# Kernel optimization log

Measured on AMD Instinct MI355X. Metric: run time of the kernel, lower is better.

The kernel has to match this reference:

```python
import jax, jax.numpy as jnp
import numpy as np

HIDDEN = 2048
N_HEADS = 32
N_KV = 8
HEAD_DIM = HIDDEN // N_HEADS
SEQ = 2048
BATCH = 1
THETA = 10000.0
EPS = 1e-5


def _layernorm(x, g, b):
    mu = jnp.mean(x, axis=-1, keepdims=True)
    var = jnp.var(x, axis=-1, keepdims=True)
    return (x - mu) * jax.lax.rsqrt(var + EPS) * g + b


def _rope_tables(seq_len, dim, theta):
    inv_freq = 1.0 / (theta ** (jnp.arange(0, dim, 2, dtype=jnp.float32) / dim))
    t = jnp.arange(seq_len, dtype=jnp.float32)
    freqs = jnp.einsum('i,j->ij', t, inv_freq)          # [S, D/2]
    emb = jnp.concatenate([freqs, freqs], axis=-1)       # [S, D]
    return jnp.cos(emb), jnp.sin(emb)


def _rotate_half(x):
    x1, x2 = jnp.split(x, 2, axis=-1)
    return jnp.concatenate([-x2, x1], axis=-1)


def setup_inputs() -> dict:
    key = jax.random.key(0)
    ks = jax.random.split(key, 10)
    s = 0.02
    return {
        'x':   jax.random.normal(ks[0], (BATCH, SEQ, HIDDEN), jnp.float32),
        'Wq':  jax.random.normal(ks[1], (HIDDEN, HIDDEN), jnp.float32) * s,
        'bq':  jnp.zeros((HIDDEN,), jnp.float32),
        'Wk':  jax.random.normal(ks[2], (HIDDEN, N_KV * HEAD_DIM), jnp.float32) * s,
        'bk':  jnp.zeros((N_KV * HEAD_DIM,), jnp.float32),
        'Wv':  jax.random.normal(ks[3], (HIDDEN, N_KV * HEAD_DIM), jnp.float32) * s,
        'bv':  jnp.zeros((N_KV * HEAD_DIM,), jnp.float32),
        'Wo':  jax.random.normal(ks[4], (HIDDEN, HIDDEN), jnp.float32) * s,
        'bo':  jnp.zeros((HIDDEN,), jnp.float32),
        'q_g': jnp.ones((HEAD_DIM,), jnp.float32),
        'q_b': jnp.zeros((HEAD_DIM,), jnp.float32),
        'k_g': jnp.ones((HEAD_DIM,), jnp.float32),
        'k_b': jnp.zeros((HEAD_DIM,), jnp.float32),
    }


def reference(x, Wq, bq, Wk, bk, Wv, bv, Wo, bo, q_g, q_b, k_g, k_b):
    B, S, H = x.shape
    n_rep = N_HEADS // N_KV
    # projections
    q = (x @ Wq + bq).reshape(B, S, N_HEADS, HEAD_DIM).transpose(0, 2, 1, 3)  # [B,Hq,S,D]
    k = (x @ Wk + bk).reshape(B, S, N_KV, HEAD_DIM).transpose(0, 2, 1, 3)     # [B,Hkv,S,D]
    v = (x @ Wv + bv).reshape(B, S, N_KV, HEAD_DIM).transpose(0, 2, 1, 3)
    # per-head QK layernorm
    q = _layernorm(q, q_g, q_b)
    k = _layernorm(k, k_g, k_b)
    # RoPE
    cos, sin = _rope_tables(S, HEAD_DIM, THETA)  # [S, D]
    q = q * cos + _rotate_half(q) * sin
    k = k * cos + _rotate_half(k) * sin
    # GQA attention without materializing repeated k/v:
    # repeat_interleave groups adjacent q-heads per kv head -> reshape q to [B,Hkv,rep,S,D]
    qg = q.reshape(B, N_KV, n_rep, S, HEAD_DIM)
    scores = jnp.einsum('bgrqd,bgkd->bgrqk', qg, k) / jnp.sqrt(jnp.float32(HEAD_DIM))
    attn = jax.nn.softmax(scores, axis=-1)
    out = jnp.einsum('bgrqk,bgkd->bgrqd', attn, v)  # [B,Hkv,rep,S,D]
    out = out.reshape(B, N_HEADS, S, HEAD_DIM).transpose(0, 2, 1, 3).reshape(B, S, H)
    return out @ Wo + bo
```

## Files before the change

### kernel.cpp

```cpp
#include <hip/hip_runtime.h>
#include <hip/hip_bf16.h>
#include <stdint.h>

#define S_LEN 2048
#define HID   2048
#define NH    32
#define NKV   8
#define HD    64

typedef __attribute__((ext_vector_type(8))) short bf16x8;
typedef __attribute__((ext_vector_type(4))) float f32x4;
typedef __attribute__((ext_vector_type(16))) float f32x16;

__device__ __forceinline__ short f2bf(float f) {
  __hip_bfloat16 h = __float2bfloat16(f);
  return __builtin_bit_cast(short, h);
}
__device__ __forceinline__ float bf2f(short s) {
  unsigned u = ((unsigned)(unsigned short)s) << 16;
  return __builtin_bit_cast(float, u);
}
__device__ __forceinline__ int cvt_pk_bf16(float lo, float hi) {
  int r;
  asm("v_cvt_pk_bf16_f32 %0, %1, %2" : "=v"(r) : "v"(lo), "v"(hi));
  return r;
}

__global__ void cast_bf16_kernel(const float* __restrict__ in, short* __restrict__ out, int n4) {
  int i = blockIdx.x * blockDim.x + threadIdx.x;
  if (i < n4) {
    float4 v = reinterpret_cast<const float4*>(in)[i];
    short4 o;
    o.x = f2bf(v.x); o.y = f2bf(v.y); o.z = f2bf(v.z); o.w = f2bf(v.w);
    reinterpret_cast<short4*>(out)[i] = o;
  }
}

__global__ void transpose_cast_kernel(const float* __restrict__ in, short* __restrict__ out,
                                      int K, int N) {
  __shared__ float tile[64][65];
  const int k0 = blockIdx.x * 64;
  const int n0 = blockIdx.y * 64;
  const int tn = threadIdx.x & 63;
  const int t4 = threadIdx.x >> 6;
#pragma unroll
  for (int i = 0; i < 16; i++)
    tile[t4 + i * 4][tn] = in[(size_t)(k0 + t4 + i * 4) * N + n0 + tn];
  __syncthreads();
#pragma unroll
  for (int i = 0; i < 16; i++)
    out[(size_t)(n0 + t4 + i * 4) * K + k0 + tn] = f2bf(tile[tn][t4 + i * 4]);
}

__global__ void concat_bias_kernel(const float* __restrict__ bq, const float* __restrict__ bk,
                                   const float* __restrict__ bv, float* __restrict__ out) {
  int i = blockIdx.x * blockDim.x + threadIdx.x;
  if (i < 3072) {
    float v = (i < 2048) ? bq[i] : (i < 2560 ? bk[i - 2048] : bv[i - 2560]);
    out[i] = v;
  }
}

__global__ void rope_table_kernel(float* __restrict__ ctab, float* __restrict__ stab) {
  int i = blockIdx.x * blockDim.x + threadIdx.x;
  if (i < S_LEN * 32) {
    int t = i >> 5, j = i & 31;
    float ang = (float)t * powf(10000.0f, -(float)j / 32.0f);
    ctab[i] = cosf(ang);
    stab[i] = sinf(ang);
  }
}

template <int F32OUT>
__global__ __launch_bounds__(256, 3) void gemm_v2_kernel(
    const short* __restrict__ A, const short* __restrict__ Bt,
    const float* __restrict__ bias, void* __restrict__ Cv,
    int N, int K) {
  __shared__ short Als[2][64 * 64];
  __shared__ short Bls[2][128 * 64];
  const int tid = threadIdx.x;
  const int l = tid & 63, w = tid >> 6;
  const int lg = l >> 4, lc = l & 15;
  const int wr = w >> 1, wc = w & 1;

  const int nwg = gridDim.x;
  const int cpx = nwg >> 3;
  const int swz = (blockIdx.x & 7) * cpx + (blockIdx.x >> 3);
  const int m0 = (swz & 31) << 6;
  const int n0 = (swz >> 5) << 7;

  const int NT = K >> 6;
  const f32x4 zero4 = {0.f, 0.f, 0.f, 0.f};
  f32x4 acc[2][4];
#pragma unroll
  for (int i = 0; i < 2; i++)
#pragma unroll
    for (int j = 0; j < 4; j++) acc[i][j] = zero4;

  const int lrow = l >> 3;
  const int lcol = (l & 7) << 3;

  auto stage = [&](int buf, int kt) {
    const int kofs = kt << 6;
#pragma unroll
    for (int i = 0; i < 2; i++) {
      const short* gsrc = A + (size_t)(m0 + i * 32 + (w << 3) + lrow) * K + kofs + lcol;
      __builtin_amdgcn_global_load_lds(
          (const __attribute__((address_space(1))) unsigned*)gsrc,
          (__attribute__((address_space(3))) unsigned*)(&Als[buf][(i * 32 + (w << 3)) << 6]),
          16, 0, 0);
    }
#pragma unroll
    for (int i = 0; i < 4; i++) {
      const short* gsrc = Bt + (size_t)(n0 + i * 32 + (w << 3) + lrow) * K + kofs + lcol;
      __builtin_amdgcn_global_load_lds(
          (const __attribute__((address_space(1))) unsigned*)gsrc,
          (__attribute__((address_space(3))) unsigned*)(&Bls[buf][(i * 32 + (w << 3)) << 6]),
          16, 0, 0);
    }
  };

  stage(0, 0);
  int cur = 0;
  for (int kt = 0; kt < NT; kt++) {
    __syncthreads();
    if (kt + 1 < NT) stage(cur ^ 1, kt + 1);
    const char* AB = reinterpret_cast<const char*>(Als[cur]);
    const char* BB = reinterpret_cast<const char*>(Bls[cur]);
#pragma unroll
    for (int ks = 0; ks < 2; ks++) {
      bf16x8 af[2], bfr[4];
#pragma unroll
      for (int mi = 0; mi < 2; mi++)
        af[mi] = *reinterpret_cast<const bf16x8*>(
            AB + (wr * 32 + mi * 16 + lc) * 128 + ks * 64 + lg * 16);
#pragma unroll
      for (int nf = 0; nf < 4; nf++)
        bfr[nf] = *reinterpret_cast<const bf16x8*>(
            BB + (wc * 64 + nf * 16 + lc) * 128 + ks * 64 + lg * 16);
#pragma unroll
      for (int mi = 0; mi < 2; mi++)
#pragma unroll
        for (int nf = 0; nf < 4; nf++)
          acc[mi][nf] = __builtin_amdgcn_mfma_f32_16x16x32_bf16(af[mi], bfr[nf], acc[mi][nf], 0, 0, 0);
    }
    cur ^= 1;
  }

#pragma unroll
  for (int mi = 0; mi < 2; mi++) {
#pragma unroll
    for (int nf = 0; nf < 4; nf++) {
      int col = n0 + wc * 64 + nf * 16 + lc;
      float bv = bias[col];
#pragma unroll
      for (int r = 0; r < 4; r++) {
        int rowg = m0 + wr * 32 + mi * 16 + lg * 4 + r;
        float v = acc[mi][nf][r] + bv;
        if (F32OUT)
          reinterpret_cast<float*>(Cv)[(size_t)rowg * N + col] = v;
        else
          reinterpret_cast<short*>(Cv)[(size_t)rowg * N + col] = f2bf(v);
      }
    }
  }
}

__global__ void ln_rope_kernel(const short* __restrict__ In, int instride, int nh_shift,
                               const float* __restrict__ gam, const float* __restrict__ bet,
                               const float* __restrict__ ctab, const float* __restrict__ stab,
                               float scale, short* __restrict__ Out) {
  const int lane = threadIdx.x & 63;
  const int nh = 1 << nh_shift;
  const int nrows = S_LEN << nh_shift;
  int row = (blockIdx.x * blockDim.x + threadIdx.x) >> 6;
  const int step = (gridDim.x * blockDim.x) >> 6;
  const float g = gam[lane], b = bet[lane];
  for (; row < nrows; row += step) {
    const int t = row >> nh_shift;
    const int h = row & (nh - 1);
    float x = bf2f(In[(size_t)t * instride + h * HD + lane]);
    float s = x;
#pragma unroll
    for (int m = 32; m >= 1; m >>= 1) s += __shfl_xor(s, m);
    const float mu = s * (1.0f / 64.0f);
    float d = x - mu;
    float v2 = d * d;
#pragma unroll
    for (int m = 32; m >= 1; m >>= 1) v2 += __shfl_xor(v2, m);
    const float var = v2 * (1.0f / 64.0f);
    float y = d * rsqrtf(var + 1e-5f) * g + b;
    float part = __shfl_xor(y, 32);
    const float c = ctab[t * 32 + (lane & 31)];
    const float sn = stab[t * 32 + (lane & 31)];
    float o = (lane < 32) ? (y * c - part * sn) : (y * c + part * sn);
    Out[((size_t)h * S_LEN + t) * HD + lane] = f2bf(o * scale);
  }
}

__global__ void v_transpose_kernel(const short* __restrict__ In, short* __restrict__ Vt) {
  __shared__ short tile[64][66];
  const int g = blockIdx.x;
  const int t0 = blockIdx.y * 64;
  const int lane = threadIdx.x & 63, w = threadIdx.x >> 6;
#pragma unroll
  for (int i = 0; i < 16; i++) {
    int r = i * 4 + w;
    tile[r][lane] = In[(size_t)(t0 + r) * 3072 + g * 64 + lane];
  }
  __syncthreads();
#pragma unroll
  for (int i = 0; i < 16; i++) {
    int d = i * 4 + w;
    Vt[((size_t)g * 64 + d) * 2048 + t0 + lane] = tile[lane][d];
  }
}

__global__ __launch_bounds__(512) void attn_kernel(
    const short* __restrict__ Q, const short* __restrict__ Kk,
    const short* __restrict__ Vt, short* __restrict__ AO) {
  __shared__ short Kls[64 * 64];
  __shared__ short Vls[64 * 64];
  const int tid = threadIdx.x;
  const int l = tid & 63;
  const int w = tid >> 6;
  const int q31 = l & 31;
  const int h = l >> 5;
  const int head = blockIdx.x;
  const int g = head >> 2;
  const int q0 = blockIdx.y * 256 + w * 32;

  bf16x8 qf[4];
  {
    const short* qb = Q + ((size_t)head * S_LEN + q0 + q31) * HD;
#pragma unroll
    for (int ks = 0; ks < 4; ks++)
      qf[ks] = *reinterpret_cast<const bf16x8*>(qb + ks * 16 + h * 8);
  }

  f32x16 oacc[2];
#pragma unroll
  for (int df = 0; df < 2; df++)
#pragma unroll
    for (int r = 0; r < 16; r++) oacc[df][r] = 0.f;
  float m_run = -1e30f, l_run = 0.f;

  const int srow = tid >> 3;
  const int kb = (tid & 7) << 4;
  const int kbs = kb ^ ((srow & 7) << 4);
  int4 kr, vr;
  auto stage_load = [&](int kt) {
    kr = *reinterpret_cast<const int4*>(Kk + ((size_t)g * S_LEN + kt * 64 + srow) * HD + (kb >> 1));
    vr = *reinterpret_cast<const int4*>(Vt + ((size_t)g * HD + srow) * S_LEN + kt * 64 + (kb >> 1));
  };
  stage_load(0);

  const int swz = (l & 7) << 4;
  const char* KB = reinterpret_cast<const char*>(Kls);
  const char* VB = reinterpret_cast<const char*>(Vls);

  for (int kt = 0; kt < S_LEN / 64; kt++) {
    __syncthreads();
    *reinterpret_cast<int4*>(reinterpret_cast<char*>(Kls) + srow * 128 + kbs) = kr;
    *reinterpret_cast<int4*>(reinterpret_cast<char*>(Vls) + srow * 128 + kbs) = vr;
    if (kt + 1 < S_LEN / 64) stage_load(kt + 1);
    __syncthreads();

    f32x16 sc[2];
#pragma unroll
    for (int i = 0; i < 16; i++) { sc[0][i] = 0.f; sc[1][i] = 0.f; }
#pragma unroll
    for (int ks = 0; ks < 4; ks++) {
#pragma unroll
      for (int kc = 0; kc < 2; kc++) {
        int row = kc * 32 + q31;
        bf16x8 kf = *reinterpret_cast<const bf16x8*>(KB + row * 128 + ((ks * 32 + h * 16) ^ swz));
        sc[kc] = __builtin_amdgcn_mfma_f32_32x32x16_bf16(kf, qf[ks], sc[kc], 0, 0, 0);
      }
    }

    float pm = sc[0][0];
#pragma unroll
    for (int kc = 0; kc < 2; kc++)
#pragma unroll
      for (int r = 0; r < 16; r++) pm = fmaxf(pm, sc[kc][r]);
    pm = fmaxf(pm, __shfl_xor(pm, 32));
    if (!__all(pm - m_run <= 11.5f)) {
      float mn = fmaxf(m_run, pm);
      float fac = __builtin_exp2f(m_run - mn);
      l_run *= fac;
#pragma unroll
      for (int df = 0; df < 2; df++)
#pragma unroll
        for (int r = 0; r < 16; r++) oacc[df][r] *= fac;
      m_run = mn;
    }
    float ps = 0.f;
#pragma unroll
    for (int kc = 0; kc < 2; kc++)
#pragma unroll
      for (int r = 0; r < 16; r++) {
        float p = __builtin_exp2f(sc[kc][r] - m_run);
        sc[kc][r] = p;
        ps += p;
      }
    ps += __shfl_xor(ps, 32);
    l_run += ps;

    bf16x8 pa[4];
#pragma unroll
    for (int c = 0; c < 4; c++) {
      const int b0 = (c & 1) * 8;
      int wa = cvt_pk_bf16(sc[c >> 1][b0 + 0], sc[c >> 1][b0 + 1]);
      int wb = cvt_pk_bf16(sc[c >> 1][b0 + 4], sc[c >> 1][b0 + 5]);
      asm volatile("v_permlane32_swap_b32 %0, %1" : "+v"(wa), "+v"(wb));
      int wc2 = cvt_pk_bf16(sc[c >> 1][b0 + 2], sc[c >> 1][b0 + 3]);
      int wd = cvt_pk_bf16(sc[c >> 1][b0 + 6], sc[c >> 1][b0 + 7]);
      asm volatile("v_permlane32_swap_b32 %0, %1" : "+v"(wc2), "+v"(wd));
      int4 pw;
      pw.x = wa; pw.y = wc2; pw.z = wb; pw.w = wd;
      pa[c] = __builtin_bit_cast(bf16x8, pw);
    }

#pragma unroll
    for (int df = 0; df < 2; df++) {
#pragma unroll
      for (int c = 0; c < 4; c++) {
        int row = df * 32 + q31;
        bf16x8 vf = *reinterpret_cast<const bf16x8*>(VB + row * 128 + ((c * 32 + h * 16) ^ swz));
        oacc[df] = __builtin_amdgcn_mfma_f32_32x32x16_bf16(vf, pa[c], oacc[df], 0, 0, 0);
      }
    }
  }

  float inv = 1.0f / l_run;
  short* aob = AO + (size_t)(q0 + q31) * HID + head * HD;
#pragma unroll
  for (int df = 0; df < 2; df++) {
#pragma unroll
    for (int rq = 0; rq < 4; rq++) {
      int v0 = cvt_pk_bf16(oacc[df][rq * 4 + 0] * inv, oacc[df][rq * 4 + 1] * inv);
      int v1 = cvt_pk_bf16(oacc[df][rq * 4 + 2] * inv, oacc[df][rq * 4 + 3] * inv);
      int2 st;
      st.x = v0; st.y = v1;
      *reinterpret_cast<int2*>(aob + df * 32 + rq * 8 + h * 4) = st;
    }
  }
}

extern "C" void kernel_launch(void* const* d_in, const int* in_sizes, int n_in,
                              void* d_out, int out_size, void* d_ws, size_t ws_size,
                              hipStream_t stream) {
  const float* x  = (const float*)d_in[0];
  const float* Wq = (const float*)d_in[1];
  const float* bq = (const float*)d_in[2];
  const float* Wk = (const float*)d_in[3];
  const float* bk = (const float*)d_in[4];
  const float* Wv = (const float*)d_in[5];
  const float* bv = (const float*)d_in[6];
  const float* Wo = (const float*)d_in[7];
  const float* bo = (const float*)d_in[8];
  const float* qg = (const float*)d_in[9];
  const float* qb = (const float*)d_in[10];
  const float* kg = (const float*)d_in[11];
  const float* kb2 = (const float*)d_in[12];
  float* out = (float*)d_out;

  char* ws = (char*)d_ws;
  size_t off = 0;
  auto alloc = [&](size_t bytes) {
    void* p = ws + off;
    off += (bytes + 255) & ~(size_t)255;
    return p;
  };
  short* xb    = (short*)alloc((size_t)2048 * 2048 * 2);
  short* Wqkvt = (short*)alloc((size_t)3072 * 2048 * 2);
  short* Wot   = (short*)alloc((size_t)2048 * 2048 * 2);
  short* QKVp  = (short*)alloc((size_t)2048 * 3072 * 2);
  short* Qr    = (short*)alloc((size_t)NH * 2048 * 64 * 2);
  short* Kr    = (short*)alloc((size_t)NKV * 2048 * 64 * 2);
  short* Vt    = (short*)alloc((size_t)NKV * 64 * 2048 * 2);
  short* AO    = (short*)alloc((size_t)2048 * 2048 * 2);
  float* ctab  = (float*)alloc((size_t)2048 * 32 * 4);
  float* stab  = (float*)alloc((size_t)2048 * 32 * 4);
  float* bqkv  = (float*)alloc((size_t)3072 * 4);

  cast_bf16_kernel<<<(2048 * 2048 / 4 + 255) / 256, 256, 0, stream>>>(x, xb, 2048 * 2048 / 4);
  transpose_cast_kernel<<<dim3(32, 32), 256, 0, stream>>>(Wq, Wqkvt, 2048, 2048);
  transpose_cast_kernel<<<dim3(32, 8), 256, 0, stream>>>(Wk, Wqkvt + (size_t)2048 * 2048, 2048, 512);
  transpose_cast_kernel<<<dim3(32, 8), 256, 0, stream>>>(Wv, Wqkvt + (size_t)2560 * 2048, 2048, 512);
  transpose_cast_kernel<<<dim3(32, 32), 256, 0, stream>>>(Wo, Wot, 2048, 2048);
  concat_bias_kernel<<<12, 256, 0, stream>>>(bq, bk, bv, bqkv);
  rope_table_kernel<<<256, 256, 0, stream>>>(ctab, stab);

  gemm_v2_kernel<0><<<768, 256, 0, stream>>>(xb, Wqkvt, bqkv, QKVp, 3072, 2048);

  ln_rope_kernel<<<512, 256, 0, stream>>>(QKVp, 3072, 5, qg, qb, ctab, stab, 0.125f * 1.44269504089f, Qr);
  ln_rope_kernel<<<256, 256, 0, stream>>>(QKVp + 2048, 3072, 3, kg, kb2, ctab, stab, 1.0f, Kr);
  v_transpose_kernel<<<dim3(8, 32), 256, 0, stream>>>(QKVp + 2560, Vt);

  attn_kernel<<<dim3(NH, 8), 512, 0, stream>>>(Qr, Kr, Vt, AO);

  gemm_v2_kernel<1><<<512, 256, 0, stream>>>(AO, Wot, bo, out, 2048, 2048);
}
```

Baseline: 316.5 us.

## Split attention into smaller 4-wave blocks, add MFMA priority hints and max3 reduction

The attention kernel now uses 256-thread blocks covering 128 query rows and launches twice as many blocks (32x16). Each thread stages two K/V rows per tile so the shared tile is still filled. s_setprio raises wave priority around the MFMA sections, and v_max3 replaces the chain of fmaxf in the row-max reduction. The aim is better load balance and occupancy across CUs and overlap of MFMA with softmax work across waves. The cost is that each K/V tile is loaded twice as often overall, since fewer waves share each tile.

```diff
diff --git a/kernel.cpp b/kernel.cpp
--- a/kernel.cpp
+++ b/kernel.cpp
@@ -23,6 +23,11 @@
 __device__ __forceinline__ int cvt_pk_bf16(float lo, float hi) {
   int r;
   asm("v_cvt_pk_bf16_f32 %0, %1, %2" : "=v"(r) : "v"(lo), "v"(hi));
+  return r;
+}
+__device__ __forceinline__ float max3f(float a, float b, float c) {
+  float r;
+  asm("v_max3_f32 %0, %1, %2, %3" : "=v"(r) : "v"(a), "v"(b), "v"(c));
   return r;
 }
 
@@ -216,7 +221,7 @@
   }
 }
 
-__global__ __launch_bounds__(512) void attn_kernel(
+__global__ __launch_bounds__(256) void attn_kernel(
     const short* __restrict__ Q, const short* __restrict__ Kk,
     const short* __restrict__ Vt, short* __restrict__ AO) {
   __shared__ short Kls[64 * 64];
@@ -228,7 +233,7 @@
   const int h = l >> 5;
   const int head = blockIdx.x;
   const int g = head >> 2;
-  const int q0 = blockIdx.y * 256 + w * 32;
+  const int q0 = blockIdx.y * 128 + w * 32;
 
   bf16x8 qf[4];
   {
@@ -248,10 +253,14 @@
   const int srow = tid >> 3;
   const int kb = (tid & 7) << 4;
   const int kbs = kb ^ ((srow & 7) << 4);
-  int4 kr, vr;
+  int4 kr[2], vr[2];
   auto stage_load = [&](int kt) {
-    kr = *reinterpret_cast<const int4*>(Kk + ((size_t)g * S_LEN + kt * 64 + srow) * HD + (kb >> 1));
-    vr = *reinterpret_cast<const int4*>(Vt + ((size_t)g * HD + srow) * S_LEN + kt * 64 + (kb >> 1));
+#pragma unroll
+    for (int c = 0; c < 2; c++) {
+      int row = c * 32 + srow;
+      kr[c] = *reinterpret_cast<const int4*>(Kk + ((size_t)g * S_LEN + kt * 64 + row) * HD + (kb >> 1));
+      vr[c] = *reinterpret_cast<const int4*>(Vt + ((size_t)g * HD + row) * S_LEN + kt * 64 + (kb >> 1));
+    }
   };
   stage_load(0);
 
@@ -261,14 +270,19 @@
 
   for (int kt = 0; kt < S_LEN / 64; kt++) {
     __syncthreads();
-    *reinterpret_cast<int4*>(reinterpret_cast<char*>(Kls) + srow * 128 + kbs) = kr;
-    *reinterpret_cast<int4*>(reinterpret_cast<char*>(Vls) + srow * 128 + kbs) = vr;
+#pragma unroll
+    for (int c = 0; c < 2; c++) {
+      int row = c * 32 + srow;
+      *reinterpret_cast<int4*>(reinterpret_cast<char*>(Kls) + row * 128 + kbs) = kr[c];
+      *reinterpret_cast<int4*>(reinterpret_cast<char*>(Vls) + row * 128 + kbs) = vr[c];
+    }
     if (kt + 1 < S_LEN / 64) stage_load(kt + 1);
     __syncthreads();
 
     f32x16 sc[2];
 #pragma unroll
     for (int i = 0; i < 16; i++) { sc[0][i] = 0.f; sc[1][i] = 0.f; }
+    __builtin_amdgcn_s_setprio(1);
 #pragma unroll
     for (int ks = 0; ks < 4; ks++) {
 #pragma unroll
@@ -278,12 +292,15 @@
         sc[kc] = __builtin_amdgcn_mfma_f32_32x32x16_bf16(kf, qf[ks], sc[kc], 0, 0, 0);
       }
     }
-
-    float pm = sc[0][0];
-#pragma unroll
-    for (int kc = 0; kc < 2; kc++)
-#pragma unroll
-      for (int r = 0; r < 16; r++) pm = fmaxf(pm, sc[kc][r]);
+    __builtin_amdgcn_s_setprio(0);
+
+    float pm = max3f(sc[0][0], sc[0][1], sc[0][2]);
+#pragma unroll
+    for (int r = 3; r < 15; r += 2) pm = max3f(pm, sc[0][r], sc[0][r + 1]);
+    pm = fmaxf(pm, sc[0][15]);
+#pragma unroll
+    for (int r = 0; r < 15; r += 2) pm = max3f(pm, sc[1][r], sc[1][r + 1]);
+    pm = fmaxf(pm, sc[1][15]);
     pm = fmaxf(pm, __shfl_xor(pm, 32));
     if (!__all(pm - m_run <= 11.5f)) {
       float mn = fmaxf(m_run, pm);
@@ -322,6 +339,7 @@
       pa[c] = __builtin_bit_cast(bf16x8, pw);
     }
 
+    __builtin_amdgcn_s_setprio(1);
 #pragma unroll
     for (int df = 0; df < 2; df++) {
 #pragma unroll
@@ -331,6 +349,7 @@
         oacc[df] = __builtin_amdgcn_mfma_f32_32x32x16_bf16(vf, pa[c], oacc[df], 0, 0, 0);
       }
     }
+    __builtin_amdgcn_s_setprio(0);
   }
 
   float inv = 1.0f / l_run;
@@ -399,7 +418,7 @@
   ln_rope_kernel<<<256, 256, 0, stream>>>(QKVp + 2048, 3072, 3, kg, kb2, ctab, stab, 1.0f, Kr);
   v_transpose_kernel<<<dim3(8, 32), 256, 0, stream>>>(QKVp + 2560, Vt);
 
-  attn_kernel<<<dim3(NH, 8), 512, 0, stream>>>(Qr, Kr, Vt, AO);
+  attn_kernel<<<dim3(NH, 16), 256, 0, stream>>>(Qr, Kr, Vt, AO);
 
   gemm_v2_kernel<1><<<512, 256, 0, stream>>>(AO, Wot, bo, out, 2048, 2048);
 }
```

After: 343.8 us. +8.6%, slower.
